# Optimization experiments

Hardware: AMD Instinct MI355X
Metric: run time of the kernel (lower is better)

Reference implementation:

```python
import jax, jax.numpy as jnp
import numpy as np

EPS = 1e-6

def _layernorm(x, g, b):
    mu = jnp.mean(x, axis=-1, keepdims=True)
    var = jnp.mean(jnp.square(x - mu), axis=-1, keepdims=True)
    return (x - mu) * jax.lax.rsqrt(var + EPS) * g + b

def setup_inputs() -> dict:
    key = jax.random.key(0)
    ks = jax.random.split(key, 5)
    B, S, C = 8, 4096, 2048
    M = 2048  # mid_channels must equal channels (norm2 shape constraint)
    x = jax.random.normal(ks[0], (B, S, C), dtype=jnp.float32)
    w1 = jax.random.normal(ks[1], (C, M), dtype=jnp.float32) * (1.0 / np.sqrt(C))
    b1 = jnp.zeros((M,), dtype=jnp.float32)
    w2 = jax.random.normal(ks[2], (M, C), dtype=jnp.float32) * (1.0 / np.sqrt(M))
    b2 = jnp.zeros((C,), dtype=jnp.float32)
    g1 = jnp.ones((C,), dtype=jnp.float32)
    be1 = jnp.zeros((C,), dtype=jnp.float32)
    g2 = jnp.ones((M,), dtype=jnp.float32)
    be2 = jnp.zeros((M,), dtype=jnp.float32)
    return {"x": x, "w1": w1, "b1": b1, "w2": w2, "b2": b2,
            "g1": g1, "be1": be1, "g2": g2, "be2": be2}

def reference(x, w1, b1, w2, b2, g1, be1, g2, be2):
    h = _layernorm(x, g1, be1)
    h = jax.nn.silu(h)
    h = jnp.einsum('bsc,cm->bsm', h, w1) + b1
    h = _layernorm(h, g2, be2)
    h = jax.nn.silu(h)
    # dropout is identity in eval mode
    h = jnp.einsum('bsm,mc->bsc', h, w2) + b2
    return x + h
```

## Files before the change

### kernel.cpp

```cpp
#include <hip/hip_runtime.h>
#include <hip/hip_bf16.h>
#include <stdint.h>

#define NROWS 32768
#define KDIM  2048
#define MDIM  2048

typedef __attribute__((ext_vector_type(8))) __bf16 bf16x8;
typedef __attribute__((ext_vector_type(4))) __bf16 bf16x4;
typedef __attribute__((ext_vector_type(4))) float  f32x4;

__device__ __forceinline__ void gload16(const __bf16* g, __bf16* l) {
    __builtin_amdgcn_global_load_lds(
        (__attribute__((address_space(1))) void*)(g),
        (__attribute__((address_space(3))) void*)(l), 16, 0, 0);
}

__global__ __launch_bounds__(256) void wsplit(const float* __restrict__ W,
                                              __bf16* __restrict__ th,
                                              __bf16* __restrict__ tl) {
    __shared__ float tile[32][33];
    const int bx = blockIdx.x & 63;
    const int by = blockIdx.x >> 6;
    const int tx = threadIdx.x & 31;
    const int ty = threadIdx.x >> 5;
#pragma unroll
    for (int i = 0; i < 32; i += 8)
        tile[ty + i][tx] = W[(size_t)(by * 32 + ty + i) * MDIM + bx * 32 + tx];
    __syncthreads();
#pragma unroll
    for (int i = 0; i < 32; i += 8) {
        const int m = bx * 32 + ty + i;
        const int k = by * 32 + tx;
        const float v = tile[tx][ty + i];
        const __bf16 hb = (__bf16)v;
        const __bf16 lb = (__bf16)(v - (float)hb);
        th[(size_t)m * KDIM + k] = hb;
        tl[(size_t)m * KDIM + k] = lb;
    }
}

__global__ __launch_bounds__(256) void ln_silu(const float* __restrict__ in,
                                               const float* __restrict__ g,
                                               const float* __restrict__ beta,
                                               __bf16* __restrict__ hi) {
    const int row  = blockIdx.x;
    const int tid  = threadIdx.x;
    const int lane = tid & 63;
    const int wv   = tid >> 6;
    const float* rp = in + (size_t)row * KDIM;

    const float4 v0 = ((const float4*)rp)[tid];
    const float4 v1 = ((const float4*)rp)[tid + 256];

    float s = v0.x + v0.y + v0.z + v0.w + v1.x + v1.y + v1.z + v1.w;
    float q = v0.x * v0.x + v0.y * v0.y + v0.z * v0.z + v0.w * v0.w +
              v1.x * v1.x + v1.y * v1.y + v1.z * v1.z + v1.w * v1.w;

#pragma unroll
    for (int off = 32; off > 0; off >>= 1) {
        s += __shfl_xor(s, off, 64);
        q += __shfl_xor(q, off, 64);
    }
    __shared__ float red[8];
    if (lane == 0) { red[wv] = s; red[4 + wv] = q; }
    __syncthreads();
    s = red[0] + red[1] + red[2] + red[3];
    q = red[4] + red[5] + red[6] + red[7];

    const float mu   = s * (1.0f / KDIM);
    const float var  = q * (1.0f / KDIM) - mu * mu;
    const float rstd = rsqrtf(var + 1e-6f);

    auto emit = [&](float4 v, int c0) {
        bf16x4 h4;
        const float xs[4] = {v.x, v.y, v.z, v.w};
#pragma unroll
        for (int j = 0; j < 4; j++) {
            const int c = c0 + j;
            const float t  = (xs[j] - mu) * rstd * g[c] + beta[c];
            const float sv = t / (1.0f + __expf(-t));
            h4[j] = (__bf16)sv;
        }
        *(bf16x4*)(hi + (size_t)row * KDIM + c0) = h4;
    };
    emit(v0, tid * 4);
    emit(v1, 1024 + tid * 4);
}

__global__ __launch_bounds__(256, 2) void gemm2p(
        const __bf16* __restrict__ Ah,
        const __bf16* __restrict__ Bh, const __bf16* __restrict__ Bl,
        const float* __restrict__ bias, const float* __restrict__ res,
        float* __restrict__ out) {
    __shared__ __align__(16) __bf16 sAh[128 * 32];
    __shared__ __align__(16) __bf16 sBh[128 * 32];
    __shared__ __align__(16) __bf16 sBl[128 * 32];

    const int tid  = threadIdx.x;
    const int lane = tid & 63;
    const int wv   = tid >> 6;
    const int wr   = wv >> 1;
    const int wc   = wv & 1;
    const int ml   = lane & 15;
    const int qk   = lane >> 4;

    const int bx = blockIdx.x;
    const int m0 = (bx >> 4) * 128;
    const int n0 = (bx & 15) * 128;

    const int ch   = wv * 2;
    const int srow = lane >> 2;
    const int skof = (lane & 3) * 8;

    f32x4 acc[4][4] = {};

    for (int kb = 0; kb < KDIM; kb += 32) {
#pragma unroll
        for (int qq = 0; qq < 2; qq++) {
            const int r    = (ch + qq) * 16 + srow;
            const int lofs = (ch + qq) * 512;
            const size_t ga = (size_t)(m0 + r) * KDIM + kb + skof;
            const size_t gb = (size_t)(n0 + r) * KDIM + kb + skof;
            gload16(Ah + ga, sAh + lofs);
            gload16(Bh + gb, sBh + lofs);
            gload16(Bl + gb, sBl + lofs);
        }
        __syncthreads();

        bf16x8 ah[4];
#pragma unroll
        for (int mi = 0; mi < 4; mi++) {
            const int ao = (wr * 64 + mi * 16 + ml) * 32 + qk * 8;
            ah[mi] = *(const bf16x8*)&sAh[ao];
        }
#pragma unroll
        for (int ni = 0; ni < 4; ni++) {
            const int bo = (wc * 64 + ni * 16 + ml) * 32 + qk * 8;
            const bf16x8 bh = *(const bf16x8*)&sBh[bo];
            const bf16x8 bl = *(const bf16x8*)&sBl[bo];
#pragma unroll
            for (int mi = 0; mi < 4; mi++) {
                acc[mi][ni] = __builtin_amdgcn_mfma_f32_16x16x32_bf16(ah[mi], bh, acc[mi][ni], 0, 0, 0);
                acc[mi][ni] = __builtin_amdgcn_mfma_f32_16x16x32_bf16(ah[mi], bl, acc[mi][ni], 0, 0, 0);
            }
        }
        __syncthreads();
    }

#pragma unroll
    for (int mi = 0; mi < 4; mi++) {
        const int gm = m0 + wr * 64 + mi * 16 + qk * 4;
#pragma unroll
        for (int ni = 0; ni < 4; ni++) {
            const int gn = n0 + wc * 64 + ni * 16 + ml;
            const float bv = bias[gn];
#pragma unroll
            for (int r = 0; r < 4; r++) {
                const size_t idx = (size_t)(gm + r) * MDIM + gn;
                float v = acc[mi][ni][r] + bv;
                if (res) v += res[idx];
                out[idx] = v;
            }
        }
    }
}

extern "C" void kernel_launch(void* const* d_in, const int* in_sizes, int n_in,
                              void* d_out, int out_size, void* d_ws, size_t ws_size,
                              hipStream_t stream) {
    const float* x   = (const float*)d_in[0];
    const float* w1  = (const float*)d_in[1];
    const float* b1  = (const float*)d_in[2];
    const float* w2  = (const float*)d_in[3];
    const float* b2  = (const float*)d_in[4];
    const float* g1  = (const float*)d_in[5];
    const float* be1 = (const float*)d_in[6];
    const float* g2  = (const float*)d_in[7];
    const float* be2 = (const float*)d_in[8];
    float* out = (float*)d_out;

    char* ws = (char*)d_ws;
    const size_t PLANE = (size_t)NROWS * KDIM * 2;
    const size_t WPL   = (size_t)KDIM * MDIM * 2;
    __bf16* Ah  = (__bf16*)(ws);
    __bf16* B1h = (__bf16*)(ws + PLANE);
    __bf16* B1l = (__bf16*)(ws + PLANE + WPL);
    __bf16* B2h = (__bf16*)(ws + PLANE + 2 * WPL);
    __bf16* B2l = (__bf16*)(ws + PLANE + 3 * WPL);

    wsplit<<<4096, 256, 0, stream>>>(w1, B1h, B1l);
    wsplit<<<4096, 256, 0, stream>>>(w2, B2h, B2l);

    ln_silu<<<NROWS, 256, 0, stream>>>(x, g1, be1, Ah);
    gemm2p<<<(NROWS / 128) * (MDIM / 128), 256, 0, stream>>>(
        Ah, B1h, B1l, b1, nullptr, out);

    ln_silu<<<NROWS, 256, 0, stream>>>(out, g2, be2, Ah);
    gemm2p<<<(NROWS / 128) * (MDIM / 128), 256, 0, stream>>>(
        Ah, B2h, B2l, b2, x, out);
}
```

Measured before the change: 1.735 ms.

## Rewrite GEMM as 256x256 tile, 8-wave, multi-buffered pipelined kernel with swizzled LDS

Replaces the 128x128 single-buffered GEMM with a 256x256 tile kernel using 8 waves. A is triple-buffered and B double-buffered in LDS, prefetches are interleaved between MFMA phases, and s_setprio is raised around the MFMA bursts. LDS columns are XOR-swizzled to avoid bank conflicts, and block IDs are remapped for L2 locality. The goal is to hide global-load latency and raise MFMA utilisation. The cost is more LDS and register pressure, plus fragile hand-written waitcnt and barrier logic.

```diff
diff --git a/kernel.cpp b/kernel.cpp
--- a/kernel.cpp
+++ b/kernel.cpp
@@ -88,77 +88,165 @@
     emit(v1, 1024 + tid * 4);
 }
 
-__global__ __launch_bounds__(256, 2) void gemm2p(
+#define PB   8192
+#define BOFF 24576
+#define NT   (KDIM / 32)
+
+#define MM(ACC, A_, H_, L_)                                                    \
+    ACC = __builtin_amdgcn_mfma_f32_16x16x32_bf16(A_, H_, ACC, 0, 0, 0);       \
+    ACC = __builtin_amdgcn_mfma_f32_16x16x32_bf16(A_, L_, ACC, 0, 0, 0)
+
+#define PHASE_PRE()                                                            \
+    __builtin_amdgcn_s_barrier();                                              \
+    asm volatile("s_waitcnt lgkmcnt(0)" ::: "memory");                         \
+    __builtin_amdgcn_sched_barrier(0);                                         \
+    __builtin_amdgcn_s_setprio(1)
+
+#define PHASE_POST()                                                           \
+    __builtin_amdgcn_s_setprio(0);                                             \
+    __builtin_amdgcn_s_barrier()
+
+__global__ __launch_bounds__(512, 2) void gemm8p(
         const __bf16* __restrict__ Ah,
         const __bf16* __restrict__ Bh, const __bf16* __restrict__ Bl,
         const float* __restrict__ bias, const float* __restrict__ res,
         float* __restrict__ out) {
-    __shared__ __align__(16) __bf16 sAh[128 * 32];
-    __shared__ __align__(16) __bf16 sBh[128 * 32];
-    __shared__ __align__(16) __bf16 sBl[128 * 32];
+    __shared__ __align__(16) __bf16 lds[57344];
 
     const int tid  = threadIdx.x;
     const int lane = tid & 63;
     const int wv   = tid >> 6;
-    const int wr   = wv >> 1;
-    const int wc   = wv & 1;
+    const int wr   = wv >> 2;
+    const int wc   = wv & 3;
     const int ml   = lane & 15;
     const int qk   = lane >> 4;
 
-    const int bx = blockIdx.x;
-    const int m0 = (bx >> 4) * 128;
-    const int n0 = (bx & 15) * 128;
-
-    const int ch   = wv * 2;
-    const int srow = lane >> 2;
-    const int skof = (lane & 3) * 8;
-
-    f32x4 acc[4][4] = {};
-
-    for (int kb = 0; kb < KDIM; kb += 32) {
-#pragma unroll
-        for (int qq = 0; qq < 2; qq++) {
-            const int r    = (ch + qq) * 16 + srow;
-            const int lofs = (ch + qq) * 512;
-            const size_t ga = (size_t)(m0 + r) * KDIM + kb + skof;
-            const size_t gb = (size_t)(n0 + r) * KDIM + kb + skof;
-            gload16(Ah + ga, sAh + lofs);
-            gload16(Bh + gb, sBh + lofs);
-            gload16(Bl + gb, sBl + lofs);
-        }
-        __syncthreads();
-
-        bf16x8 ah[4];
-#pragma unroll
-        for (int mi = 0; mi < 4; mi++) {
-            const int ao = (wr * 64 + mi * 16 + ml) * 32 + qk * 8;
-            ah[mi] = *(const bf16x8*)&sAh[ao];
-        }
-#pragma unroll
-        for (int ni = 0; ni < 4; ni++) {
-            const int bo = (wc * 64 + ni * 16 + ml) * 32 + qk * 8;
-            const bf16x8 bh = *(const bf16x8*)&sBh[bo];
-            const bf16x8 bl = *(const bf16x8*)&sBl[bo];
-#pragma unroll
-            for (int mi = 0; mi < 4; mi++) {
-                acc[mi][ni] = __builtin_amdgcn_mfma_f32_16x16x32_bf16(ah[mi], bh, acc[mi][ni], 0, 0, 0);
-                acc[mi][ni] = __builtin_amdgcn_mfma_f32_16x16x32_bf16(ah[mi], bl, acc[mi][ni], 0, 0, 0);
-            }
-        }
-        __syncthreads();
-    }
-
-#pragma unroll
-    for (int mi = 0; mi < 4; mi++) {
-        const int gm = m0 + wr * 64 + mi * 16 + qk * 4;
-#pragma unroll
-        for (int ni = 0; ni < 4; ni++) {
-            const int gn = n0 + wc * 64 + ni * 16 + ml;
+    const int bid = blockIdx.x;
+    const int g   = (bid & 7) * 128 + (bid >> 3);
+    const int m0  = (g & 127) * 256;
+    const int n0  = (g >> 7) * 256;
+
+    const int srow = wv * 16 + (lane >> 2);
+    const int scol = ((lane & 3) ^ ((lane >> 3) & 3)) * 8;
+    const __bf16* pA0 = Ah + (size_t)(m0 + srow) * KDIM + scol;
+    const __bf16* pA1 = Ah + (size_t)(m0 + 128 + srow) * KDIM + scol;
+    const __bf16* pH0 = Bh + (size_t)(n0 + srow) * KDIM + scol;
+    const __bf16* pH1 = Bh + (size_t)(n0 + 128 + srow) * KDIM + scol;
+    const __bf16* pL0 = Bl + (size_t)(n0 + srow) * KDIM + scol;
+    const __bf16* pL1 = Bl + (size_t)(n0 + 128 + srow) * KDIM + scol;
+    const int ld0 = wv * 512;
+    const int ld1 = 4096 + wv * 512;
+
+    const int cofs = (qk ^ ((ml >> 1) & 3)) * 8;
+    const int aoff = (wr * 128 + ml) * 32 + cofs;
+    const int boff = (wc * 64 + ml) * 32 + cofs;
+
+    f32x4 acc[8][4] = {};
+
+    gload16(pH0, lds + BOFF + ld0);
+    gload16(pH1, lds + BOFF + ld1);
+    gload16(pL0, lds + BOFF + PB + ld0);
+    gload16(pL1, lds + BOFF + PB + ld1);
+    gload16(pA0, lds + ld0);
+    gload16(pA1, lds + ld1);
+    gload16(pA0 + 32, lds + PB + ld0);
+    gload16(pA1 + 32, lds + PB + ld1);
+    asm volatile("s_waitcnt vmcnt(2)" ::: "memory");
+    __builtin_amdgcn_sched_barrier(0);
+    __builtin_amdgcn_s_barrier();
+
+    int ta = 0;
+    int pa = 2;
+    for (int t = 0; t < NT; ++t) {
+        __bf16* const aB = lds + ta * PB;
+        __bf16* const hB = lds + BOFF + (t & 1) * 2 * PB;
+        __bf16* const lB = hB + PB;
+        __bf16* const hN = lds + BOFF + ((t + 1) & 1) * 2 * PB;
+        const bool pfB = (t + 1) < NT;
+        const bool pfA = (t + 2) < NT;
+        const int  kB  = (t + 1) * 32;
+        const int  kA  = (t + 2) * 32;
+
+        bf16x8 a0, a1, a2, a3, h0, h1, h2, h3, l0, l1, l2, l3;
+
+        a0 = *(const bf16x8*)(aB + aoff);
+        a1 = *(const bf16x8*)(aB + aoff + 512);
+        a2 = *(const bf16x8*)(aB + aoff + 1024);
+        a3 = *(const bf16x8*)(aB + aoff + 1536);
+        h0 = *(const bf16x8*)(hB + boff);
+        h1 = *(const bf16x8*)(hB + boff + 512);
+        l0 = *(const bf16x8*)(lB + boff);
+        l1 = *(const bf16x8*)(lB + boff + 512);
+        if (pfB) {
+            gload16(pH0 + kB, hN + ld0);
+            gload16(pH1 + kB, hN + ld1);
+        }
+        PHASE_PRE();
+        MM(acc[0][0], a0, h0, l0); MM(acc[1][0], a1, h0, l0);
+        MM(acc[2][0], a2, h0, l0); MM(acc[3][0], a3, h0, l0);
+        MM(acc[0][1], a0, h1, l1); MM(acc[1][1], a1, h1, l1);
+        MM(acc[2][1], a2, h1, l1); MM(acc[3][1], a3, h1, l1);
+        PHASE_POST();
+
+        h2 = *(const bf16x8*)(hB + boff + 1024);
+        h3 = *(const bf16x8*)(hB + boff + 1536);
+        l2 = *(const bf16x8*)(lB + boff + 1024);
+        l3 = *(const bf16x8*)(lB + boff + 1536);
+        if (pfB) {
+            gload16(pL0 + kB, hN + PB + ld0);
+            gload16(pL1 + kB, hN + PB + ld1);
+        }
+        PHASE_PRE();
+        MM(acc[0][2], a0, h2, l2); MM(acc[1][2], a1, h2, l2);
+        MM(acc[2][2], a2, h2, l2); MM(acc[3][2], a3, h2, l2);
+        MM(acc[0][3], a0, h3, l3); MM(acc[1][3], a1, h3, l3);
+        MM(acc[2][3], a2, h3, l3); MM(acc[3][3], a3, h3, l3);
+        PHASE_POST();
+
+        a0 = *(const bf16x8*)(aB + aoff + 2048);
+        a1 = *(const bf16x8*)(aB + aoff + 2560);
+        a2 = *(const bf16x8*)(aB + aoff + 3072);
+        a3 = *(const bf16x8*)(aB + aoff + 3584);
+        if (pfA) {
+            gload16(pA0 + kA, lds + pa * PB + ld0);
+            gload16(pA1 + kA, lds + pa * PB + ld1);
+        }
+        PHASE_PRE();
+        MM(acc[4][2], a0, h2, l2); MM(acc[5][2], a1, h2, l2);
+        MM(acc[6][2], a2, h2, l2); MM(acc[7][2], a3, h2, l2);
+        MM(acc[4][3], a0, h3, l3); MM(acc[5][3], a1, h3, l3);
+        MM(acc[6][3], a2, h3, l3); MM(acc[7][3], a3, h3, l3);
+        PHASE_POST();
+
+        PHASE_PRE();
+        MM(acc[4][0], a0, h0, l0); MM(acc[5][0], a1, h0, l0);
+        MM(acc[6][0], a2, h0, l0); MM(acc[7][0], a3, h0, l0);
+        MM(acc[4][1], a0, h1, l1); MM(acc[5][1], a1, h1, l1);
+        MM(acc[6][1], a2, h1, l1); MM(acc[7][1], a3, h1, l1);
+        __builtin_amdgcn_s_setprio(0);
+        if (pfA) {
+            asm volatile("s_waitcnt vmcnt(2)" ::: "memory");
+        } else if (pfB) {
+            asm volatile("s_waitcnt vmcnt(0)" ::: "memory");
+        }
+        __builtin_amdgcn_sched_barrier(0);
+        if (pfB) __builtin_amdgcn_s_barrier();
+
+        ta = (ta == 2) ? 0 : ta + 1;
+        pa = (pa == 2) ? 0 : pa + 1;
+    }
+
+#pragma unroll
+    for (int i = 0; i < 8; i++) {
+        const int gm = m0 + wr * 128 + (i >> 2) * 64 + (i & 3) * 16 + qk * 4;
+#pragma unroll
+        for (int j = 0; j < 4; j++) {
+            const int gn = n0 + wc * 64 + j * 16 + ml;
             const float bv = bias[gn];
 #pragma unroll
             for (int r = 0; r < 4; r++) {
                 const size_t idx = (size_t)(gm + r) * MDIM + gn;
-                float v = acc[mi][ni][r] + bv;
+                float v = acc[i][j][r] + bv;
                 if (res) v += res[idx];
                 out[idx] = v;
             }
@@ -183,7 +271,7 @@
     char* ws = (char*)d_ws;
     const size_t PLANE = (size_t)NROWS * KDIM * 2;
     const size_t WPL   = (size_t)KDIM * MDIM * 2;
-    __bf16* Ah  = (__bf16*)(ws);
+    __bf16* Ahp = (__bf16*)(ws);
     __bf16* B1h = (__bf16*)(ws + PLANE);
     __bf16* B1l = (__bf16*)(ws + PLANE + WPL);
     __bf16* B2h = (__bf16*)(ws + PLANE + 2 * WPL);
@@ -192,11 +280,11 @@
     wsplit<<<4096, 256, 0, stream>>>(w1, B1h, B1l);
     wsplit<<<4096, 256, 0, stream>>>(w2, B2h, B2l);
 
-    ln_silu<<<NROWS, 256, 0, stream>>>(x, g1, be1, Ah);
-    gemm2p<<<(NROWS / 128) * (MDIM / 128), 256, 0, stream>>>(
-        Ah, B1h, B1l, b1, nullptr, out);
-
-    ln_silu<<<NROWS, 256, 0, stream>>>(out, g2, be2, Ah);
-    gemm2p<<<(NROWS / 128) * (MDIM / 128), 256, 0, stream>>>(
-        Ah, B2h, B2l, b2, x, out);
-}
+    ln_silu<<<NROWS, 256, 0, stream>>>(x, g1, be1, Ahp);
+    gemm8p<<<(NROWS / 256) * (MDIM / 256), 512, 0, stream>>>(
+        Ahp, B1h, B1l, b1, nullptr, out);
+
+    ln_silu<<<NROWS, 256, 0, stream>>>(out, g2, be2, Ahp);
+    gemm8p<<<(NROWS / 256) * (MDIM / 256), 512, 0, stream>>>(
+        Ahp, B2h, B2l, b2, x, out);
+}
```

Result: faster. 1.654 ms (-4.7%).
